# Performance work log

Measured on AMD Instinct MI355X. Metric: run time of the kernel, lower is better.

The kernel has to match this reference:

```python
import jax, jax.numpy as jnp
import numpy as np

B, S, D = 2, 2048, 1024
N_QK, N_V, N_KNOW = 4096, 4096, 8192
N_HEADS = 16
MAX_K_QK, MAX_K_V, MAX_K_KNOW = 32, 32, 64
LN_EPS = 1e-6


def _unit_norm(key, shape, scale=1.0):
    x = jax.random.normal(key, shape, jnp.float32)
    return x / (jnp.linalg.norm(x, axis=-1, keepdims=True) + 1e-8) * scale


def setup_inputs() -> dict:
    key = jax.random.key(0)
    ks = jax.random.split(key, 12)
    return {
        "x": jax.random.normal(ks[0], (B, S, D), jnp.float32),
        "qk_emb": _unit_norm(ks[1], (N_QK, D)),
        "qk_w": _unit_norm(ks[2], (N_QK, D)),
        "v_emb": _unit_norm(ks[3], (N_V, D)),
        "v_w": _unit_norm(ks[4], (N_V, D)),
        "know_emb": _unit_norm(ks[5], (N_KNOW, D)),
        "know_w": _unit_norm(ks[6], (N_KNOW, D)),
        "tau_attn_k": jax.random.normal(ks[7], (D, 3), jnp.float32) * (1.0 / np.sqrt(D)),
        "tau_attn_b": jnp.zeros((3,), jnp.float32),
        "tau_know_k": jax.random.normal(ks[8], (D, 1), jnp.float32) * (1.0 / np.sqrt(D)),
        "tau_know_b": jnp.zeros((1,), jnp.float32),
        "expand_O": jax.random.normal(ks[9], (D, D), jnp.float32) * 0.02,
        "ln1_scale": jnp.ones((D,), jnp.float32),
        "ln1_bias": jnp.zeros((D,), jnp.float32),
        "ln2_scale": jnp.ones((D,), jnp.float32),
        "ln2_bias": jnp.zeros((D,), jnp.float32),
    }


def _layer_norm(x, scale, bias):
    mean = jnp.mean(x, axis=-1, keepdims=True)
    var = jnp.mean(jnp.square(x - mean), axis=-1, keepdims=True)
    return (x - mean) / jnp.sqrt(var + LN_EPS) * scale + bias


def threshold_gate(scores, tau, max_k):
    # scores: [B,S,N], tau: [B,S,1]
    raw = scores - tau
    gate = jnp.where(raw > 0, raw, 1e-8 * jnp.exp(raw))
    exp_gate = jnp.exp(gate) - 1.0
    topk_vals, _ = jax.lax.top_k(exp_gate, min(max_k, scores.shape[-1]))
    thr = topk_vals[:, :, -1:]
    exp_gate = jnp.where(exp_gate >= thr, exp_gate, 0.0)
    gate_sum = exp_gate.sum(axis=-1, keepdims=True) + 1e-8
    strength = jnp.tanh(exp_gate.max(axis=-1, keepdims=True))
    return exp_gate / gate_sum * strength


@jax.checkpoint
def sense_emit_full(x, emb, w, gate):
    # [B,S,D] @ [D,N] -> gated [B,S,N] -> [B,S,D]
    return ((x @ emb.T) * gate) @ w


def _block(x, qk_emb, qk_w, v_emb, v_w, know_emb, know_w,
           tau_attn_k, tau_attn_b, tau_know_k, tau_know_b,
           expand_O, ln1_scale, ln1_bias, ln2_scale, ln2_bias):
    # ---- attention circuit (deterministic; dropout = identity) ----
    normed = _layer_norm(x, ln1_scale, ln1_bias)
    scores_qk = normed @ qk_emb.T           # [B,S,N_QK]
    scores_v = normed @ v_emb.T             # [B,S,N_V]
    tau_all = normed @ tau_attn_k + tau_attn_b  # [B,S,3]
    g_Q = threshold_gate(scores_qk, tau_all[:, :, 0:1], MAX_K_QK)
    g_K = threshold_gate(scores_qk, tau_all[:, :, 1:2], MAX_K_QK)
    g_V = threshold_gate(scores_v, tau_all[:, :, 2:3], MAX_K_V)
    t_qk = 1.0 / qk_emb.shape[0]
    t_v = 1.0 / v_emb.shape[0]
    a_aux = (((g_Q.mean(axis=(0, 1)) - t_qk) ** 2).sum() * g_Q.shape[-1]
             + ((g_K.mean(axis=(0, 1)) - t_qk) ** 2).sum() * g_K.shape[-1]
             + ((g_V.mean(axis=(0, 1)) - t_v) ** 2).sum() * g_V.shape[-1])

    Q = sense_emit_full(normed, qk_emb, qk_w, g_Q)
    K = sense_emit_full(normed, qk_emb, qk_w, g_K)
    V = sense_emit_full(normed, v_emb, v_w, g_V)

    Bs, Ss, Ds = x.shape
    d_head = Ds // N_HEADS
    Q = Q.reshape(Bs, Ss, N_HEADS, d_head).transpose(0, 2, 1, 3)
    K = K.reshape(Bs, Ss, N_HEADS, d_head).transpose(0, 2, 1, 3)
    V = V.reshape(Bs, Ss, N_HEADS, d_head).transpose(0, 2, 1, 3)
    scale = jnp.sqrt(jnp.float32(d_head))
    attn = jnp.einsum('bhsd,bhtd->bhst', Q, K) / scale
    causal = jnp.tril(jnp.ones((Ss, Ss), dtype=jnp.bool_))
    attn = jnp.where(causal, attn, jnp.finfo(attn.dtype).min)
    attn = jax.nn.softmax(attn, axis=-1)
    out = jnp.einsum('bhst,bhtd->bhsd', attn, V)
    out = out.transpose(0, 2, 1, 3).reshape(Bs, Ss, Ds)
    out = out @ expand_O
    x = x + out

    # ---- knowledge circuit ----
    normed = _layer_norm(x, ln2_scale, ln2_bias)
    scores_k = normed @ know_emb.T          # [B,S,N_KNOW]
    tau_k = normed @ tau_know_k + tau_know_b
    gate = threshold_gate(scores_k, tau_k, MAX_K_KNOW)
    t_k = 1.0 / know_emb.shape[0]
    k_aux = ((gate.mean(axis=(0, 1)) - t_k) ** 2).sum() * know_emb.shape[0]
    know_out = sense_emit_full(normed, know_emb, know_w, gate)
    x = x + know_out
    return x, a_aux + k_aux


def reference(x, qk_emb, qk_w, v_emb, v_w, know_emb, know_w,
              tau_attn_k, tau_attn_b, tau_know_k, tau_know_b,
              expand_O, ln1_scale, ln1_bias, ln2_scale, ln2_bias):
    return _block(x, qk_emb, qk_w, v_emb, v_w, know_emb, know_w,
                  tau_attn_k, tau_attn_b, tau_know_k, tau_know_b,
                  expand_O, ln1_scale, ln1_bias, ln2_scale, ln2_bias)
```

## Files before the change

### kernel.cpp

```cpp
#include <hip/hip_runtime.h>

#define TOK   4096
#define DIM   1024
#define NQK   4096
#define NV    4096
#define NKN   8192
#define SLEN  2048
#define NH    16
#define DH    64
#define CAPA  48
#define CAPK  96
#define APAD  72

typedef float  f32x4  __attribute__((ext_vector_type(4)));
typedef short  short8 __attribute__((ext_vector_type(8)));
typedef unsigned int  u32;
typedef unsigned short u16;

__device__ __forceinline__ u16 f2bf(float f) {
    u32 u = __float_as_uint(f);
    u32 r = (u + 0x7fffu + ((u >> 16) & 1u)) >> 16;
    return (u16)r;
}
__device__ __forceinline__ float bf2f(u16 v) { return __uint_as_float(((u32)v) << 16); }

__device__ __forceinline__ u16 bfkey(u16 b) {
    return (b & 0x8000u) ? (u16)(~b) : (u16)(b | 0x8000u);
}
__device__ __forceinline__ u16 keybf(u16 k) {
    return (k & 0x8000u) ? (u16)(k & 0x7fffu) : (u16)(~k);
}

__device__ __forceinline__ f32x4 mfma_bf16(short8 a, short8 b, f32x4 c) {
    asm volatile("v_mfma_f32_16x16x32_bf16 %0, %1, %2, %0"
                 : "+v"(c) : "v"(a), "v"(b));
    return c;
}

__device__ __forceinline__ void gload16(const u16* g, u16* s) {
    __builtin_amdgcn_global_load_lds((const __attribute__((address_space(1))) void*)g,
                                     (__attribute__((address_space(3))) void*)s, 16, 0, 0);
}

__device__ __forceinline__ float blockReduceF(float v, float* red, int wave, int lane) {
#pragma unroll
    for (int off = 32; off > 0; off >>= 1) v += __shfl_xor(v, off);
    __syncthreads();
    if (lane == 0) red[wave] = v;
    __syncthreads();
    return red[0] + red[1] + red[2] + red[3];
}

__global__ __launch_bounds__(256) void k_convert_all(const float* __restrict__ p0,
                                                     const float* __restrict__ p1,
                                                     const float* __restrict__ p2,
                                                     const float* __restrict__ p3,
                                                     const float* __restrict__ p4,
                                                     const float* __restrict__ p5,
                                                     u16* __restrict__ o0, u16* __restrict__ o1,
                                                     u16* __restrict__ o2, u16* __restrict__ o3,
                                                     u16* __restrict__ o4, u16* __restrict__ o5) {
    const int S0 = 1048576, S1 = 2097152, S2 = 4194304, S3 = 5242880, S4 = 6291456, S5 = 8388608;
    for (int i = blockIdx.x * 256 + threadIdx.x; i < S5; i += gridDim.x * 256) {
        const float* in; u16* out; int off;
        if (i < S0)      { in = p0; out = o0; off = i; }
        else if (i < S1) { in = p1; out = o1; off = i - S0; }
        else if (i < S2) { in = p2; out = o2; off = i - S1; }
        else if (i < S3) { in = p3; out = o3; off = i - S2; }
        else if (i < S4) { in = p4; out = o4; off = i - S3; }
        else             { in = p5; out = o5; off = i - S4; }
        float4 v = reinterpret_cast<const float4*>(in)[off];
        reinterpret_cast<ushort4*>(out)[off] = make_ushort4(f2bf(v.x), f2bf(v.y), f2bf(v.z), f2bf(v.w));
    }
}

__global__ __launch_bounds__(256) void k_transpose_bf16(const float* __restrict__ in,
                                                        u16* __restrict__ out) {
    __shared__ float tile[32][33];
    int bx = blockIdx.x * 32;
    int by = blockIdx.y * 32;
    int tx = threadIdx.x & 31;
    int ty = threadIdx.x >> 5;
    for (int r = ty; r < 32; r += 8)
        tile[r][tx] = in[(size_t)(by + r) * DIM + bx + tx];
    __syncthreads();
    for (int r = ty; r < 32; r += 8)
        out[(size_t)(bx + r) * DIM + by + tx] = f2bf(tile[tx][r]);
}

__global__ __launch_bounds__(256) void k_ln_tau(const float* __restrict__ x,
                                                const float* __restrict__ sc,
                                                const float* __restrict__ bi,
                                                const float* __restrict__ tauk,
                                                const float* __restrict__ taub,
                                                int ntau,
                                                u16* __restrict__ nrm,
                                                float* __restrict__ tau_out) {
    __shared__ float red[4];
    int t = blockIdx.x, tid = threadIdx.x, wave = tid >> 6, lane = tid & 63;
    const float4 xv = reinterpret_cast<const float4*>(x + (size_t)t * DIM)[tid];
    float s = xv.x + xv.y + xv.z + xv.w;
    s = blockReduceF(s, red, wave, lane);
    float mean = s * (1.0f / DIM);
    float d0 = xv.x - mean, d1 = xv.y - mean, d2 = xv.z - mean, d3 = xv.w - mean;
    float ss = d0 * d0 + d1 * d1 + d2 * d2 + d3 * d3;
    ss = blockReduceF(ss, red, wave, lane);
    float rstd = rsqrtf(ss * (1.0f / DIM) + 1e-6f);
    const float4 scv = reinterpret_cast<const float4*>(sc)[tid];
    const float4 biv = reinterpret_cast<const float4*>(bi)[tid];
    float n0 = d0 * rstd * scv.x + biv.x;
    float n1 = d1 * rstd * scv.y + biv.y;
    float n2 = d2 * rstd * scv.z + biv.z;
    float n3 = d3 * rstd * scv.w + biv.w;
    ushort4 o = make_ushort4(f2bf(n0), f2bf(n1), f2bf(n2), f2bf(n3));
    reinterpret_cast<ushort4*>(nrm + (size_t)t * DIM)[tid] = o;
    int d = tid * 4;
    for (int j = 0; j < ntau; j++) {
        float p = n0 * tauk[(size_t)(d + 0) * ntau + j] + n1 * tauk[(size_t)(d + 1) * ntau + j]
                + n2 * tauk[(size_t)(d + 2) * ntau + j] + n3 * tauk[(size_t)(d + 3) * ntau + j];
        p = blockReduceF(p, red, wave, lane);
        if (tid == 0) tau_out[(size_t)t * ntau + j] = p + taub[j];
    }
}

template<int TAG, int KEYOUT>
__global__ __launch_bounds__(256) void k_gemm_bt(const u16* __restrict__ A,
                                                 const u16* __restrict__ B,
                                                 void* __restrict__ Cv,
                                                 int M, int N, int K,
                                                 const float* __restrict__ res) {
    __shared__ __align__(16) u16 As[8192];
    __shared__ __align__(16) u16 Bs[8192];
    int tid = threadIdx.x;
    int wave = tid >> 6, lane = tid & 63;
    int m0 = blockIdx.y * 128, n0 = blockIdx.x * 128;
    int wm = (wave >> 1) * 64, wn = (wave & 1) * 64;
    int kg = lane >> 4, l15 = lane & 15;

    const u16* gA[4]; const u16* gB[4];
    u16* sA[4]; u16* sB[4];
#pragma unroll
    for (int i = 0; i < 4; i++) {
        int c = wave * 4 + i;
        int cs = c >> 1, h = c & 1;
        gA[i] = A + (size_t)(m0 + h * 64 + lane) * K + cs * 8;
        gB[i] = B + (size_t)(n0 + h * 64 + lane) * K + cs * 8;
        sA[i] = As + cs * 1024 + h * 512;
        sB[i] = Bs + cs * 1024 + h * 512;
    }

    f32x4 acc[4][4];
#pragma unroll
    for (int i = 0; i < 4; i++)
#pragma unroll
        for (int j = 0; j < 4; j++) { f32x4 z = {0.f, 0.f, 0.f, 0.f}; acc[i][j] = z; }

    for (int k0 = 0; k0 < K; k0 += 64) {
        __syncthreads();
#pragma unroll
        for (int i = 0; i < 4; i++) {
            gload16(gA[i] + k0, sA[i]);
            gload16(gB[i] + k0, sB[i]);
        }
        __syncthreads();
#pragma unroll
        for (int ks = 0; ks < 2; ks++) {
            int cso = (ks * 4 + kg) * 1024;
            short8 af[4], bg[4];
#pragma unroll
            for (int mi = 0; mi < 4; mi++)
                af[mi] = *reinterpret_cast<const short8*>(&As[cso + (wm + mi * 16 + l15) * 8]);
#pragma unroll
            for (int ni = 0; ni < 4; ni++)
                bg[ni] = *reinterpret_cast<const short8*>(&Bs[cso + (wn + ni * 16 + l15) * 8]);
#pragma unroll
            for (int mi = 0; mi < 4; mi++)
#pragma unroll
                for (int ni = 0; ni < 4; ni++)
                    acc[mi][ni] = mfma_bf16(af[mi], bg[ni], acc[mi][ni]);
        }
    }
    asm volatile("s_nop 7\n\ts_nop 7");
#pragma unroll
    for (int mi = 0; mi < 4; mi++) {
#pragma unroll
        for (int ni = 0; ni < 4; ni++) {
            int col = n0 + wn + ni * 16 + l15;
#pragma unroll
            for (int r = 0; r < 4; r++) {
                int rowm = m0 + wm + mi * 16 + (lane >> 4) * 4 + r;
                size_t idx = (size_t)rowm * N + col;
                float v = acc[mi][ni][r];
                if (KEYOUT) {
                    ((u16*)Cv)[idx] = bfkey(f2bf(v));
                } else {
                    if (res) v += res[idx];
                    ((float*)Cv)[idx] = v;
                }
            }
        }
    }
}

template<int TWO, int RES>
__global__ __launch_bounds__(256) void k_gate_emit(const u16* __restrict__ keys_g, int ldk,
                                                   int NC, int ksel, int row_off,
                                                   const float* __restrict__ tau, int tau_stride, int tcol0,
                                                   const u16* __restrict__ w,
                                                   u16* __restrict__ OA, u16* __restrict__ OB,
                                                   float* __restrict__ io,
                                                   float* __restrict__ csA, float* __restrict__ csB) {
    extern __shared__ u16 keys[];
    __shared__ int   hist[256];
    __shared__ int   scnt;
    __shared__ int   dsel;
    __shared__ int   knext;
    __shared__ int   sidx[CAPK];
    __shared__ float svA[CAPK];
    __shared__ float svB[CAPK];
    int r = blockIdx.x, tid = threadIdx.x, wave = tid >> 6, lane = tid & 63;
    int t = row_off + r;
    const int cap = TWO ? CAPA : (RES ? CAPK : CAPA);

    const uint4* srow8 = reinterpret_cast<const uint4*>(keys_g + (size_t)r * ldk);
    for (int c = tid; c < NC / 8; c += 256)
        reinterpret_cast<uint4*>(keys)[c] = srow8[c];
    if (tid == 0) scnt = 0;

    u32 prefix = 0;
    int krem = ksel;
#pragma unroll
    for (int pass = 0; pass < 2; pass++) {
        int shift = 8 - pass * 8;
        hist[tid] = 0;
        __syncthreads();
        u32 pmask = (pass == 0) ? 0u : 0xFF00u;
        for (int i = tid; i < NC; i += 256) {
            u32 ky = keys[i];
            if ((ky & pmask) == prefix)
                atomicAdd(&hist[(ky >> shift) & 255], 1);
        }
        __syncthreads();
        int v = hist[tid];
#pragma unroll
        for (int off = 1; off < 256; off <<= 1) {
            int other = (tid + off < 256) ? hist[tid + off] : 0;
            __syncthreads();
            v += other;
            hist[tid] = v;
            __syncthreads();
        }
        int sfx = v;
        int sfx_next = (tid < 255) ? hist[tid + 1] : 0;
        if (sfx >= krem && (tid == 255 || sfx_next < krem)) {
            dsel = tid;
            knext = krem - sfx_next;
        }
        __syncthreads();
        prefix |= ((u32)dsel) << shift;
        krem = knext;
        __syncthreads();
    }
    u32 thr = prefix;

    for (int i = tid; i < NC; i += 256) {
        u32 ky = keys[i];
        if (ky >= thr) {
            int p = atomicAdd(&scnt, 1);
            if (p < cap) {
                sidx[p] = i;
                svA[p] = bf2f(keybf((u16)ky));
            }
        }
    }
    __syncthreads();
    int n = scnt < cap ? scnt : cap;

    if (wave == 0) {
        float tA = tau[(size_t)t * tau_stride + tcol0];
        float tB = TWO ? tau[(size_t)t * tau_stride + tcol0 + 1] : 0.f;
        float sumA = 0.f, mxA = -1e30f, sumB = 0.f, mxB = -1e30f;
        float sv0 = (lane < n) ? svA[lane] : 0.f;
        float sv1 = (lane + 64 < n) ? svA[lane + 64] : 0.f;
        for (int i = lane; i < n; i += 64) {
            float sv = svA[i];
            float rA = sv - tA;
            float gA = rA > 0.f ? rA : 1e-8f * expf(rA);
            float eA = expf(gA) - 1.0f;
            sumA += eA; mxA = fmaxf(mxA, eA);
            if (TWO) {
                float rB = sv - tB;
                float gB = rB > 0.f ? rB : 1e-8f * expf(rB);
                float eB = expf(gB) - 1.0f;
                sumB += eB; mxB = fmaxf(mxB, eB);
            }
        }
#pragma unroll
        for (int off = 32; off > 0; off >>= 1) {
            sumA += __shfl_xor(sumA, off); mxA = fmaxf(mxA, __shfl_xor(mxA, off));
            sumB += __shfl_xor(sumB, off); mxB = fmaxf(mxB, __shfl_xor(mxB, off));
        }
        float fA = tanhf(mxA) / (sumA + 1e-8f);
        float fB = tanhf(mxB) / (sumB + 1e-8f);
        if (lane < n) {
            float sv = sv0; int ci = sidx[lane];
            float rA = sv - tA;
            float gA = rA > 0.f ? rA : 1e-8f * expf(rA);
            float ga = (expf(gA) - 1.0f) * fA;
            svA[lane] = ga * sv;
            atomicAdd(&csA[ci], ga);
            if (TWO) {
                float rB = sv - tB;
                float gB = rB > 0.f ? rB : 1e-8f * expf(rB);
                float gb = (expf(gB) - 1.0f) * fB;
                svB[lane] = gb * sv;
                atomicAdd(&csB[ci], gb);
            }
        }
        if (lane + 64 < n) {
            float sv = sv1; int ci = sidx[lane + 64];
            float rA = sv - tA;
            float gA = rA > 0.f ? rA : 1e-8f * expf(rA);
            float ga = (expf(gA) - 1.0f) * fA;
            svA[lane + 64] = ga * sv;
            atomicAdd(&csA[ci], ga);
            if (TWO) {
                float rB = sv - tB;
                float gB = rB > 0.f ? rB : 1e-8f * expf(rB);
                float gb = (expf(gB) - 1.0f) * fB;
                svB[lane + 64] = gb * sv;
                atomicAdd(&csB[ci], gb);
            }
        }
    }
    __syncthreads();

    float a0 = 0, a1 = 0, a2 = 0, a3 = 0, b0 = 0, b1 = 0, b2 = 0, b3 = 0;
    float4 base;
    if (RES) base = reinterpret_cast<const float4*>(io + (size_t)t * DIM)[tid];
    int s = 0;
    for (; s + 4 <= n; s += 4) {
        const ushort4 w0 = reinterpret_cast<const ushort4*>(w + (size_t)sidx[s]     * DIM)[tid];
        const ushort4 w1 = reinterpret_cast<const ushort4*>(w + (size_t)sidx[s + 1] * DIM)[tid];
        const ushort4 w2 = reinterpret_cast<const ushort4*>(w + (size_t)sidx[s + 2] * DIM)[tid];
        const ushort4 w3 = reinterpret_cast<const ushort4*>(w + (size_t)sidx[s + 3] * DIM)[tid];
        float vA0 = svA[s], vA1 = svA[s + 1], vA2 = svA[s + 2], vA3 = svA[s + 3];
        a0 += vA0 * bf2f(w0.x) + vA1 * bf2f(w1.x) + vA2 * bf2f(w2.x) + vA3 * bf2f(w3.x);
        a1 += vA0 * bf2f(w0.y) + vA1 * bf2f(w1.y) + vA2 * bf2f(w2.y) + vA3 * bf2f(w3.y);
        a2 += vA0 * bf2f(w0.z) + vA1 * bf2f(w1.z) + vA2 * bf2f(w2.z) + vA3 * bf2f(w3.z);
        a3 += vA0 * bf2f(w0.w) + vA1 * bf2f(w1.w) + vA2 * bf2f(w2.w) + vA3 * bf2f(w3.w);
        if (TWO) {
            float vB0 = svB[s], vB1 = svB[s + 1], vB2 = svB[s + 2], vB3 = svB[s + 3];
            b0 += vB0 * bf2f(w0.x) + vB1 * bf2f(w1.x) + vB2 * bf2f(w2.x) + vB3 * bf2f(w3.x);
            b1 += vB0 * bf2f(w0.y) + vB1 * bf2f(w1.y) + vB2 * bf2f(w2.y) + vB3 * bf2f(w3.y);
            b2 += vB0 * bf2f(w0.z) + vB1 * bf2f(w1.z) + vB2 * bf2f(w2.z) + vB3 * bf2f(w3.z);
            b3 += vB0 * bf2f(w0.w) + vB1 * bf2f(w1.w) + vB2 * bf2f(w2.w) + vB3 * bf2f(w3.w);
        }
    }
    for (; s < n; s++) {
        const ushort4 wv = reinterpret_cast<const ushort4*>(w + (size_t)sidx[s] * DIM)[tid];
        float va = svA[s];
        a0 += va * bf2f(wv.x); a1 += va * bf2f(wv.y); a2 += va * bf2f(wv.z); a3 += va * bf2f(wv.w);
        if (TWO) {
            float vb = svB[s];
            b0 += vb * bf2f(wv.x); b1 += vb * bf2f(wv.y); b2 += vb * bf2f(wv.z); b3 += vb * bf2f(wv.w);
        }
    }
    if (RES) {
        reinterpret_cast<float4*>(io + (size_t)t * DIM)[tid] =
            make_float4(base.x + a0, base.y + a1, base.z + a2, base.w + a3);
    } else {
        reinterpret_cast<ushort4*>(OA + (size_t)t * DIM)[tid] = make_ushort4(f2bf(a0), f2bf(a1), f2bf(a2), f2bf(a3));
        if (TWO)
            reinterpret_cast<ushort4*>(OB + (size_t)t * DIM)[tid] = make_ushort4(f2bf(b0), f2bf(b1), f2bf(b2), f2bf(b3));
    }
}

__global__ __launch_bounds__(256) void k_attn(const u16* __restrict__ Q,
                                              const u16* __restrict__ K,
                                              const u16* __restrict__ V,
                                              u16* __restrict__ O) {
    __shared__ __align__(16) u16 Qs[64 * APAD];
    __shared__ __align__(16) u16 Ks[64 * APAD];
    __shared__ __align__(16) u16 Vt[64 * APAD];
    __shared__ __align__(16) u16 Ps[4][16 * APAD];
    int tid = threadIdx.x, wave = tid >> 6, lane = tid & 63;
    int h = blockIdx.x, bb = blockIdx.y, qt = blockIdx.z;
    int q0 = qt * 64;
    size_t base = ((size_t)bb * SLEN) * DIM + (size_t)h * DH;
    int sr = tid >> 2, sc = (tid & 3) * 16;
    int g = lane >> 4, l15 = lane & 15;

    {
        const u16* qp = Q + base + (size_t)(q0 + sr) * DIM + sc;
        *reinterpret_cast<short8*>(&Qs[sr * APAD + sc])     = *reinterpret_cast<const short8*>(qp);
        *reinterpret_cast<short8*>(&Qs[sr * APAD + sc + 8]) = *reinterpret_cast<const short8*>(qp + 8);
    }
    __syncthreads();
    short8 qa0 = *reinterpret_cast<const short8*>(&Qs[(wave * 16 + l15) * APAD + g * 8]);
    short8 qa1 = *reinterpret_cast<const short8*>(&Qs[(wave * 16 + l15) * APAD + 32 + g * 8]);

    float m[4], l[4];
    f32x4 oacc[4];
#pragma unroll
    for (int i = 0; i < 4; i++) {
        m[i] = -1e30f; l[i] = 0.f;
        f32x4 z = {0.f, 0.f, 0.f, 0.f}; oacc[i] = z;
    }
    u16* pw = &Ps[wave][0];

    for (int kc = 0; kc <= qt; kc++) {
        __syncthreads();
        {
            const u16* kp = K + base + (size_t)(kc * 64 + sr) * DIM + sc;
            *reinterpret_cast<short8*>(&Ks[sr * APAD + sc])     = *reinterpret_cast<const short8*>(kp);
            *reinterpret_cast<short8*>(&Ks[sr * APAD + sc + 8]) = *reinterpret_cast<const short8*>(kp + 8);
            const u16* vp = V + base + (size_t)(kc * 64 + sr) * DIM + sc;
            short8 w0 = *reinterpret_cast<const short8*>(vp);
            short8 w1 = *reinterpret_cast<const short8*>(vp + 8);
            const u16* w0p = reinterpret_cast<const u16*>(&w0);
            const u16* w1p = reinterpret_cast<const u16*>(&w1);
#pragma unroll
            for (int j = 0; j < 16; j++) {
                int d = sc + j;
                int phys = (((sr >> 3) + d + (d >> 4)) & 7);
                Vt[d * APAD + phys * 8 + (sr & 7)] = (j < 8) ? w0p[j] : w1p[j - 8];
            }
        }
        __syncthreads();

        f32x4 s4[4];
#pragma unroll
        for (int ks = 0; ks < 4; ks++) {
            f32x4 z = {0.f, 0.f, 0.f, 0.f}; s4[ks] = z;
            short8 kb0 = *reinterpret_cast<const short8*>(&Ks[(ks * 16 + l15) * APAD + g * 8]);
            short8 kb1 = *reinterpret_cast<const short8*>(&Ks[(ks * 16 + l15) * APAD + 32 + g * 8]);
            s4[ks] = mfma_bf16(qa0, kb0, s4[ks]);
            s4[ks] = mfma_bf16(qa1, kb1, s4[ks]);
        }
        asm volatile("s_nop 7\n\ts_nop 7");

        int key_base = kc * 64 + l15;
#pragma unroll
        for (int ks = 0; ks < 4; ks++) {
            int key = key_base + ks * 16;
#pragma unroll
            for (int r = 0; r < 4; r++) {
                int q_abs = q0 + wave * 16 + g * 4 + r;
                float sv = s4[ks][r] * 0.125f;
                s4[ks][r] = (key > q_abs) ? -1e30f : sv;
            }
        }

#pragma unroll
        for (int r = 0; r < 4; r++) {
            float mx = fmaxf(fmaxf(s4[0][r], s4[1][r]), fmaxf(s4[2][r], s4[3][r]));
            mx = fmaxf(mx, __shfl_xor(mx, 1));
            mx = fmaxf(mx, __shfl_xor(mx, 2));
            mx = fmaxf(mx, __shfl_xor(mx, 4));
            mx = fmaxf(mx, __shfl_xor(mx, 8));
            float mnew = fmaxf(m[r], mx);
            float al = __expf(m[r] - mnew);
            m[r] = mnew;
            float p0 = __expf(s4[0][r] - mnew);
            float p1 = __expf(s4[1][r] - mnew);
            float p2 = __expf(s4[2][r] - mnew);
            float p3 = __expf(s4[3][r] - mnew);
            float ps = p0 + p1 + p2 + p3;
            ps += __shfl_xor(ps, 1);
            ps += __shfl_xor(ps, 2);
            ps += __shfl_xor(ps, 4);
            ps += __shfl_xor(ps, 8);
            l[r] = l[r] * al + ps;
#pragma unroll
            for (int ds_ = 0; ds_ < 4; ds_++) oacc[ds_][r] *= al;
            int row = g * 4 + r;
            pw[row * APAD +  0 + l15] = f2bf(p0);
            pw[row * APAD + 16 + l15] = f2bf(p1);
            pw[row * APAD + 32 + l15] = f2bf(p2);
            pw[row * APAD + 48 + l15] = f2bf(p3);
        }

        short8 pa0 = *reinterpret_cast<const short8*>(&pw[l15 * APAD + g * 8]);
        short8 pa1 = *reinterpret_cast<const short8*>(&pw[l15 * APAD + 32 + g * 8]);
#pragma unroll
        for (int dsub = 0; dsub < 4; dsub++) {
            int d = dsub * 16 + l15;
            int rot = d + (d >> 4);
            short8 vb0 = *reinterpret_cast<const short8*>(&Vt[d * APAD + (((0 + g) + rot) & 7) * 8]);
            short8 vb1 = *reinterpret_cast<const short8*>(&Vt[d * APAD + (((4 + g) + rot) & 7) * 8]);
            oacc[dsub] = mfma_bf16(pa0, vb0, oacc[dsub]);
            oacc[dsub] = mfma_bf16(pa1, vb1, oacc[dsub]);
        }
    }
    asm volatile("s_nop 7\n\ts_nop 7");

#pragma unroll
    for (int r = 0; r < 4; r++) {
        float inv = 1.0f / l[r];
        int row = q0 + wave * 16 + g * 4 + r;
#pragma unroll
        for (int dsub = 0; dsub < 4; dsub++) {
            O[base + (size_t)row * DIM + dsub * 16 + l15] = f2bf(oacc[dsub][r] * inv);
        }
    }
}

__global__ __launch_bounds__(256) void k_aux(const float* __restrict__ cs,
                                             float* __restrict__ out_aux) {
    __shared__ float red[4];
    int gtid = blockIdx.x * 256 + threadIdx.x;
    float acc = 0.f;
    for (int i = gtid; i < 3 * 4096 + 8192; i += gridDim.x * 256) {
        float mean = cs[i] * (1.0f / 4096.0f);
        float tN, Nf;
        if (i < 12288) { tN = 1.0f / 4096.0f; Nf = 4096.0f; }
        else           { tN = 1.0f / 8192.0f; Nf = 8192.0f; }
        float d = mean - tN;
        acc += d * d * Nf;
    }
    acc = blockReduceF(acc, red, threadIdx.x >> 6, threadIdx.x & 63);
    if (threadIdx.x == 0) atomicAdd(out_aux, acc);
}

extern "C" void kernel_launch(void* const* d_in, const int* in_sizes, int n_in,
                              void* d_out, int out_size, void* d_ws, size_t ws_size,
                              hipStream_t stream) {
    const float* x         = (const float*)d_in[0];
    const float* qk_emb    = (const float*)d_in[1];
    const float* qk_w      = (const float*)d_in[2];
    const float* v_emb     = (const float*)d_in[3];
    const float* v_w       = (const float*)d_in[4];
    const float* know_emb  = (const float*)d_in[5];
    const float* know_w    = (const float*)d_in[6];
    const float* tau_attn_k = (const float*)d_in[7];
    const float* tau_attn_b = (const float*)d_in[8];
    const float* tau_know_k = (const float*)d_in[9];
    const float* tau_know_b = (const float*)d_in[10];
    const float* expand_O  = (const float*)d_in[11];
    const float* ln1_s     = (const float*)d_in[12];
    const float* ln1_b     = (const float*)d_in[13];
    const float* ln2_s     = (const float*)d_in[14];
    const float* ln2_b     = (const float*)d_in[15];
    float* out = (float*)d_out;
    char*  ws  = (char*)d_ws;

    u16*   nrm_bf   = (u16*)(ws + 0);
    u16*   qkemb_bf = (u16*)(ws + 8388608);
    u16*   vemb_bf  = (u16*)(ws + 16777216);
    u16*   knemb_bf = (u16*)(ws + 25165824);
    u16*   expT_bf  = (u16*)(ws + 41943040);
    u16*   attn_bf  = (u16*)(ws + 44040192);
    u16*   qkw_bf   = (u16*)(ws + 52428800);
    u16*   vw_bf    = (u16*)(ws + 60817408);
    u16*   knw_bf   = (u16*)(ws + 69206016);
    u16*   Qb       = (u16*)(ws + 85983232);
    u16*   Kb       = (u16*)(ws + 94371840);
    u16*   Vb       = (u16*)(ws + 102760448);
    u16*   keysbuf  = (u16*)(ws + 111149056);
    float* tauA     = (float*)(ws + 185384960);
    float* tauKn    = (float*)(ws + 185434112);
    float* colsum   = (float*)(ws + 185450496);
    const size_t WS_NEEDED = 185532416;
    if (ws_size < WS_NEEDED) return;

    float* colQ = colsum, *colK = colsum + 4096, *colV = colsum + 8192, *colKn = colsum + 12288;

    hipMemsetAsync(colsum, 0, 20480 * sizeof(float), stream);
    hipMemsetAsync(out + (size_t)TOK * DIM, 0, sizeof(float), stream);

    k_convert_all<<<2048, 256, 0, stream>>>(qk_emb, v_emb, know_emb, qk_w, v_w, know_w,
                                            qkemb_bf, vemb_bf, knemb_bf, qkw_bf, vw_bf, knw_bf);
    k_transpose_bf16<<<dim3(32, 32), 256, 0, stream>>>(expand_O, expT_bf);

    k_ln_tau<<<TOK, 256, 0, stream>>>(x, ln1_s, ln1_b, tau_attn_k, tau_attn_b, 3, nrm_bf, tauA);

    k_gemm_bt<0, 1><<<dim3(8192 / 128, TOK / 128), 256, 0, stream>>>(nrm_bf, qkemb_bf, keysbuf, TOK, 8192, DIM, nullptr);
    k_gate_emit<1, 0><<<TOK, 256, NQK * sizeof(u16), stream>>>(keysbuf, 8192, NQK, 32, 0, tauA, 3, 0,
                                                               qkw_bf, Qb, Kb, nullptr, colQ, colK);
    k_gate_emit<0, 0><<<TOK, 256, NV * sizeof(u16), stream>>>(keysbuf + 4096, 8192, NV, 32, 0, tauA, 3, 2,
                                                              vw_bf, Vb, nullptr, nullptr, colV, nullptr);

    k_attn<<<dim3(NH, 2, SLEN / 64), 256, 0, stream>>>(Qb, Kb, Vb, attn_bf);

    k_gemm_bt<2, 0><<<dim3(DIM / 128, TOK / 128), 256, 0, stream>>>(attn_bf, expT_bf, out, TOK, DIM, DIM, x);

    k_ln_tau<<<TOK, 256, 0, stream>>>(out, ln2_s, ln2_b, tau_know_k, tau_know_b, 1, nrm_bf, tauKn);

    k_gemm_bt<3, 1><<<dim3(NKN / 128, TOK / 128), 256, 0, stream>>>(nrm_bf, knemb_bf, keysbuf, TOK, NKN, DIM, nullptr);
    k_gate_emit<0, 1><<<TOK, 256, NKN * sizeof(u16), stream>>>(keysbuf, NKN, NKN, 64, 0, tauKn, 1, 0,
                                                               knw_bf, nullptr, nullptr, out, colKn, nullptr);

    k_aux<<<20, 256, 0, stream>>>(colsum, out + (size_t)TOK * DIM);
}
```

Before: 715.1 us.

## Replace LDS-staged GEMM with direct global-to-register MFMA operand loads

The bf16 GEMM kernel no longer stages A and B tiles through shared memory with global_load_lds and two barriers per K step. Each wave now loads its MFMA fragments straight from global memory into registers, with a 2x unrolled K loop. This removes the barriers and the LDS traffic. In exchange, data is no longer shared between waves in a block, so global/L2 traffic roughly doubles, and access is strided per row (16 bytes per lane per row), which may hurt coalescing and latency hiding.

```diff
diff --git a/kernel.cpp b/kernel.cpp
--- a/kernel.cpp
+++ b/kernel.cpp
@@ -35,11 +35,6 @@
     asm volatile("v_mfma_f32_16x16x32_bf16 %0, %1, %2, %0"
                  : "+v"(c) : "v"(a), "v"(b));
     return c;
-}
-
-__device__ __forceinline__ void gload16(const u16* g, u16* s) {
-    __builtin_amdgcn_global_load_lds((const __attribute__((address_space(1))) void*)g,
-                                     (__attribute__((address_space(3))) void*)s, 16, 0, 0);
 }
 
 __device__ __forceinline__ float blockReduceF(float v, float* red, int wave, int lane) {
@@ -124,30 +119,25 @@
 }
 
 template<int TAG, int KEYOUT>
-__global__ __launch_bounds__(256) void k_gemm_bt(const u16* __restrict__ A,
-                                                 const u16* __restrict__ B,
-                                                 void* __restrict__ Cv,
-                                                 int M, int N, int K,
-                                                 const float* __restrict__ res) {
-    __shared__ __align__(16) u16 As[8192];
-    __shared__ __align__(16) u16 Bs[8192];
+__global__ __launch_bounds__(256) void k_gemm_reg(const u16* __restrict__ A,
+                                                  const u16* __restrict__ B,
+                                                  void* __restrict__ Cv,
+                                                  int M, int N, int K,
+                                                  const float* __restrict__ res) {
     int tid = threadIdx.x;
     int wave = tid >> 6, lane = tid & 63;
     int m0 = blockIdx.y * 128, n0 = blockIdx.x * 128;
     int wm = (wave >> 1) * 64, wn = (wave & 1) * 64;
     int kg = lane >> 4, l15 = lane & 15;
 
-    const u16* gA[4]; const u16* gB[4];
-    u16* sA[4]; u16* sB[4];
-#pragma unroll
-    for (int i = 0; i < 4; i++) {
-        int c = wave * 4 + i;
-        int cs = c >> 1, h = c & 1;
-        gA[i] = A + (size_t)(m0 + h * 64 + lane) * K + cs * 8;
-        gB[i] = B + (size_t)(n0 + h * 64 + lane) * K + cs * 8;
-        sA[i] = As + cs * 1024 + h * 512;
-        sB[i] = Bs + cs * 1024 + h * 512;
-    }
+    const u16* pA[4];
+    const u16* pB[4];
+#pragma unroll
+    for (int mi = 0; mi < 4; mi++)
+        pA[mi] = A + (size_t)(m0 + wm + mi * 16 + l15) * K + kg * 8;
+#pragma unroll
+    for (int ni = 0; ni < 4; ni++)
+        pB[ni] = B + (size_t)(n0 + wn + ni * 16 + l15) * K + kg * 8;
 
     f32x4 acc[4][4];
 #pragma unroll
@@ -155,30 +145,20 @@
 #pragma unroll
         for (int j = 0; j < 4; j++) { f32x4 z = {0.f, 0.f, 0.f, 0.f}; acc[i][j] = z; }
 
-    for (int k0 = 0; k0 < K; k0 += 64) {
-        __syncthreads();
-#pragma unroll
-        for (int i = 0; i < 4; i++) {
-            gload16(gA[i] + k0, sA[i]);
-            gload16(gB[i] + k0, sB[i]);
-        }
-        __syncthreads();
-#pragma unroll
-        for (int ks = 0; ks < 2; ks++) {
-            int cso = (ks * 4 + kg) * 1024;
-            short8 af[4], bg[4];
-#pragma unroll
-            for (int mi = 0; mi < 4; mi++)
-                af[mi] = *reinterpret_cast<const short8*>(&As[cso + (wm + mi * 16 + l15) * 8]);
+#pragma unroll 2
+    for (int k0 = 0; k0 < K; k0 += 32) {
+        short8 af[4], bg[4];
+#pragma unroll
+        for (int mi = 0; mi < 4; mi++)
+            af[mi] = *reinterpret_cast<const short8*>(pA[mi] + k0);
+#pragma unroll
+        for (int ni = 0; ni < 4; ni++)
+            bg[ni] = *reinterpret_cast<const short8*>(pB[ni] + k0);
+#pragma unroll
+        for (int mi = 0; mi < 4; mi++)
 #pragma unroll
             for (int ni = 0; ni < 4; ni++)
-                bg[ni] = *reinterpret_cast<const short8*>(&Bs[cso + (wn + ni * 16 + l15) * 8]);
-#pragma unroll
-            for (int mi = 0; mi < 4; mi++)
-#pragma unroll
-                for (int ni = 0; ni < 4; ni++)
-                    acc[mi][ni] = mfma_bf16(af[mi], bg[ni], acc[mi][ni]);
-        }
+                acc[mi][ni] = mfma_bf16(af[mi], bg[ni], acc[mi][ni]);
     }
     asm volatile("s_nop 7\n\ts_nop 7");
 #pragma unroll
@@ -575,7 +555,7 @@
 
     k_ln_tau<<<TOK, 256, 0, stream>>>(x, ln1_s, ln1_b, tau_attn_k, tau_attn_b, 3, nrm_bf, tauA);
 
-    k_gemm_bt<0, 1><<<dim3(8192 / 128, TOK / 128), 256, 0, stream>>>(nrm_bf, qkemb_bf, keysbuf, TOK, 8192, DIM, nullptr);
+    k_gemm_reg<0, 1><<<dim3(8192 / 128, TOK / 128), 256, 0, stream>>>(nrm_bf, qkemb_bf, keysbuf, TOK, 8192, DIM, nullptr);
     k_gate_emit<1, 0><<<TOK, 256, NQK * sizeof(u16), stream>>>(keysbuf, 8192, NQK, 32, 0, tauA, 3, 0,
                                                                qkw_bf, Qb, Kb, nullptr, colQ, colK);
     k_gate_emit<0, 0><<<TOK, 256, NV * sizeof(u16), stream>>>(keysbuf + 4096, 8192, NV, 32, 0, tauA, 3, 2,
@@ -583,11 +563,11 @@
 
     k_attn<<<dim3(NH, 2, SLEN / 64), 256, 0, stream>>>(Qb, Kb, Vb, attn_bf);
 
-    k_gemm_bt<2, 0><<<dim3(DIM / 128, TOK / 128), 256, 0, stream>>>(attn_bf, expT_bf, out, TOK, DIM, DIM, x);
+    k_gemm_reg<2, 0><<<dim3(DIM / 128, TOK / 128), 256, 0, stream>>>(attn_bf, expT_bf, out, TOK, DIM, DIM, x);
 
     k_ln_tau<<<TOK, 256, 0, stream>>>(out, ln2_s, ln2_b, tau_know_k, tau_know_b, 1, nrm_bf, tauKn);
 
-    k_gemm_bt<3, 1><<<dim3(NKN / 128, TOK / 128), 256, 0, stream>>>(nrm_bf, knemb_bf, keysbuf, TOK, NKN, DIM, nullptr);
+    k_gemm_reg<3, 1><<<dim3(NKN / 128, TOK / 128), 256, 0, stream>>>(nrm_bf, knemb_bf, keysbuf, TOK, NKN, DIM, nullptr);
     k_gate_emit<0, 1><<<TOK, 256, NKN * sizeof(u16), stream>>>(keysbuf, NKN, NKN, 64, 0, tauKn, 1, 0,
                                                                knw_bf, nullptr, nullptr, out, colKn, nullptr);
 
```

Result: slower. 917.0 us (+28.2%).
